# Kernel optimization log

Measured on AMD Instinct MI355X. Metric: run time of the kernel, lower is better.

The kernel has to match this reference:

```python
import jax, jax.numpy as jnp
import numpy as np

B, H, L, P = 16, 256, 8192, 64  # batch, d_input, seq_len, d_state


def setup_inputs() -> dict:
    key = jax.random.key(0)
    k1, k2, k3, k4, k5, k6 = jax.random.split(key, 6)
    u = jax.random.normal(k1, (B, H, L), dtype=jnp.float32)
    # diagonal SSM poles on an annulus inside the unit disk (stable discrete dynamics)
    radius = jax.random.uniform(k2, (P,), minval=0.5, maxval=0.99)
    theta = jax.random.uniform(k3, (P,), minval=0.0, maxval=2.0 * np.pi)
    A_re = (radius * jnp.cos(theta)).astype(jnp.float32)
    A_im = (radius * jnp.sin(theta)).astype(jnp.float32)
    # combined input/output mixing W = C*B, complex (H, P)
    BC_re = (jax.random.normal(k4, (H, P)) / np.sqrt(P)).astype(jnp.float32)
    BC_im = (jax.random.normal(k5, (H, P)) / np.sqrt(P)).astype(jnp.float32)
    # D skip vector: uniform_ring(min_radius=0.0, max_radius=1.0, field='real')
    D = jax.random.uniform(k6, (H,), minval=0.0, maxval=1.0, dtype=jnp.float32)
    return {"u": u, "A_re": A_re, "A_im": A_im, "BC_re": BC_re, "BC_im": BC_im, "D": D}


def reference(u, A_re, A_im, BC_re, BC_im, D):
    # Vandermonde kernel: k[h, l] = sum_p BC[h, p] * A[p]**l, computed stably via exp(l*log A)
    A = jax.lax.complex(A_re, A_im)                      # (P,)
    logA = jnp.log(A)                                    # (P,) complex
    ell = jnp.arange(L, dtype=jnp.float32)               # (L,)
    V = jnp.exp(logA[:, None] * ell[None, :])            # (P, L) complex Vandermonde
    BC = jax.lax.complex(BC_re, BC_im)                   # (H, P)
    k = jnp.einsum('hp,pl->hl', BC, V)                   # (H, L) complex kernel
    # circular FFT convolution (same-length fft/ifft as the torch code)
    u_s = jnp.fft.fft(u, axis=-1)                        # (B, H, L) complex
    k_s = jnp.fft.fft(k, axis=-1)                        # (H, L) complex
    y = jnp.fft.ifft(u_s * k_s[None, :, :], axis=-1).real
    y = y + D[None, :, None] * u                         # D*u skip
    return jnp.tanh(y)                                   # activation (dropout=0 -> identity)
```

## Files before the change

kernel.cpp:

```cpp
#include <hip/hip_runtime.h>
#include <cmath>


typedef _Float16 half8 __attribute__((ext_vector_type(8)));
typedef _Float16 half4v __attribute__((ext_vector_type(4)));
typedef float floatx16 __attribute__((ext_vector_type(16)));

#define NC 64
#define CM 128
#define ROWP 136
#define A2_BYTES ((size_t)256 * 128 * 256 * 2)
#define W_BYTES  ((size_t)128 * 128 * 2)
#define AM_OFF   (A2_BYTES + W_BYTES)

__device__ __forceinline__ float fast_tanh(float x) {
    float e2 = __expf(2.0f * x);
    return 1.0f - 2.0f / (e2 + 1.0f);
}

__global__ void fftconv_prep(const float* __restrict__ A_re, const float* __restrict__ A_im,
                             const float* __restrict__ BC_re, const float* __restrict__ BC_im,
                             const float* __restrict__ Dv, char* __restrict__ ws) {
    __shared__ float rr[64], th[64], br[64], bi[64];
    __shared__ float kk[CM];
    const int h = blockIdx.x, tid = threadIdx.x;
    if (tid < 64) {
        float x = A_re[tid], y = A_im[tid];
        rr[tid] = log2f(sqrtf(x * x + y * y));
        th[tid] = atan2f(y, x);
        br[tid] = BC_re[h * 64 + tid];
        bi[tid] = BC_im[h * 64 + tid];
    }
    __syncthreads();
    if (tid < CM) {
        float d = (float)tid, s = 0.f;
        for (int p = 0; p < 64; ++p) {
            float mag = exp2f(d * rr[p]);
            float ang = d * th[p];
            s += mag * (br[p] * cosf(ang) - bi[p] * sinf(ang));
        }
        kk[tid] = s;
    }
    __syncthreads();
    _Float16* A2 = (_Float16*)ws + (size_t)h * 128 * 256;
    const float Dh = Dv[h];
    for (int idx = tid; idx < 128 * 128; idx += 256) {
        int r = idx >> 7, pc = idx & 127, p = pc & 63;
        float e = (float)(r + 1);
        float mag = exp2f(e * rr[p]);
        float ang = e * th[p];
        float cr = mag * cosf(ang), ci = mag * sinf(ang);
        float val = (pc < 64) ? (br[p] * cr - bi[p] * ci) : -(br[p] * ci + bi[p] * cr);
        A2[r * 256 + pc] = (_Float16)val;
    }
    for (int idx = tid; idx < 128 * 128; idx += 256) {
        int r = idx >> 7, j = idx & 127;
        float v = (j <= r) ? kk[r - j] : 0.f;
        if (j == r) v += Dh;
        A2[r * 256 + CM + j] = (_Float16)v;
    }
    if (h == 0) {
        _Float16* W = (_Float16*)(ws + A2_BYTES);
        for (int idx = tid; idx < 128 * 128; idx += 256) {
            int pc = idx >> 7, j = idx & 127, p = pc & 63;
            float e = (float)(127 - j);
            float mag = exp2f(e * rr[p]);
            float ang = e * th[p];
            float v = (pc < 64) ? mag * cosf(ang) : mag * sinf(ang);
            W[pc * 128 + j] = (_Float16)v;
        }
        if (tid < 64) {
            float mag = exp2f(128.f * rr[tid]);
            float ang = 128.f * th[tid];
            float* aM = (float*)(ws + AM_OFF);
            aM[tid] = mag * cosf(ang);
            aM[64 + tid] = mag * sinf(ang);
        }
    }
}

__global__ __launch_bounds__(256, 2)
void fftconv_main(const float* __restrict__ u, const char* __restrict__ ws,
                  float* __restrict__ out) {
    __shared__ __align__(16) _Float16 u16p[NC * ROWP];
    __shared__ __align__(16) _Float16 S16[NC * ROWP];

    const int tid = threadIdx.x;
    const int lane = tid & 63;
    const int wv = tid >> 6;
    const int h = blockIdx.x >> 4;
    const int bb = blockIdx.x & 15;
    const float* ub = u + ((size_t)bb * 256 + h) * 8192;
    float* yb = out + ((size_t)bb * 256 + h) * 8192;

#pragma unroll
    for (int i = 0; i < 8; ++i) {
        int e4 = i * 256 + tid;
        float4 v = ((const float4*)ub)[e4];
        int el = e4 << 2;
        int c = el >> 7, j = el & 127;
        half4v hv = { (_Float16)v.x, (_Float16)v.y, (_Float16)v.z, (_Float16)v.w };
        *(half4v*)&u16p[c * ROWP + j] = hv;
    }
    __syncthreads();

    const int mrow = (wv << 5) + (lane & 31);
    const int kh = (lane >> 5) << 3;
    const int ncol = lane & 31;

    {
        const _Float16* Wg = (const _Float16*)(ws + A2_BYTES);
        floatx16 acc0 = {}; floatx16 acc1 = {};
#pragma unroll
        for (int s = 0; s < 8; ++s) {
            int k0 = (s << 4) + kh;
            half8 af = *(const half8*)(Wg + mrow * CM + k0);
            half8 b0 = *(const half8*)&u16p[ncol * ROWP + k0];
            half8 b1 = *(const half8*)&u16p[(ncol + 32) * ROWP + k0];
            acc0 = __builtin_amdgcn_mfma_f32_32x32x16_f16(af, b0, acc0, 0, 0, 0);
            acc1 = __builtin_amdgcn_mfma_f32_32x32x16_f16(af, b1, acc1, 0, 0, 0);
        }
        const int pc0 = (wv << 5) + ((lane >> 5) << 2);
#pragma unroll
        for (int g = 0; g < 4; ++g) {
            half4v h0 = { (_Float16)acc0[4 * g + 0], (_Float16)acc0[4 * g + 1],
                          (_Float16)acc0[4 * g + 2], (_Float16)acc0[4 * g + 3] };
            *(half4v*)&S16[ncol * ROWP + pc0 + 8 * g] = h0;
            half4v h1 = { (_Float16)acc1[4 * g + 0], (_Float16)acc1[4 * g + 1],
                          (_Float16)acc1[4 * g + 2], (_Float16)acc1[4 * g + 3] };
            *(half4v*)&S16[(ncol + 32) * ROWP + pc0 + 8 * g] = h1;
        }
    }
    __syncthreads();

    if (wv == 0) {
        const float* aM = (const float*)(ws + AM_OFF);
        const float amr = aM[lane], ami = aM[64 + lane];
        float sr = 0.f, si = 0.f;
#pragma unroll
        for (int c = NC - 8; c < NC; ++c) {
            float xr = (float)S16[c * ROWP + lane];
            float xi = (float)S16[c * ROWP + 64 + lane];
            float nr = fmaf(amr, sr, fmaf(-ami, si, xr));
            float ni = fmaf(amr, si, fmaf(ami, sr, xi));
            sr = nr; si = ni;
        }
#pragma unroll
        for (int c = 0; c < NC; ++c) {
            float xr = (float)S16[c * ROWP + lane];
            float xi = (float)S16[c * ROWP + 64 + lane];
            S16[c * ROWP + lane] = (_Float16)sr;
            S16[c * ROWP + 64 + lane] = (_Float16)si;
            float nr = fmaf(amr, sr, fmaf(-ami, si, xr));
            float ni = fmaf(amr, si, fmaf(ami, sr, xi));
            sr = nr; si = ni;
        }
    }
    __syncthreads();

    {
        const _Float16* Ag = (const _Float16*)ws + ((size_t)h * CM + mrow) * 256;
        floatx16 acc0 = {}; floatx16 acc1 = {};
#pragma unroll
        for (int s = 0; s < 8; ++s) {
            int k0 = (s << 4) + kh;
            half8 af = *(const half8*)(Ag + k0);
            half8 b0 = *(const half8*)&S16[ncol * ROWP + k0];
            half8 b1 = *(const half8*)&S16[(ncol + 32) * ROWP + k0];
            acc0 = __builtin_amdgcn_mfma_f32_32x32x16_f16(af, b0, acc0, 0, 0, 0);
            acc1 = __builtin_amdgcn_mfma_f32_32x32x16_f16(af, b1, acc1, 0, 0, 0);
        }
#pragma unroll
        for (int s = 0; s < 8; ++s) {
            int k0 = (s << 4) + kh;
            half8 af = *(const half8*)(Ag + CM + k0);
            half8 b0 = *(const half8*)&u16p[ncol * ROWP + k0];
            half8 b1 = *(const half8*)&u16p[(ncol + 32) * ROWP + k0];
            acc0 = __builtin_amdgcn_mfma_f32_32x32x16_f16(af, b0, acc0, 0, 0, 0);
            acc1 = __builtin_amdgcn_mfma_f32_32x32x16_f16(af, b1, acc1, 0, 0, 0);
        }
        const int r0 = (wv << 5) + ((lane >> 5) << 2);
#pragma unroll
        for (int g = 0; g < 4; ++g) {
            float4 o0;
            o0.x = fast_tanh(acc0[4 * g + 0]); o0.y = fast_tanh(acc0[4 * g + 1]);
            o0.z = fast_tanh(acc0[4 * g + 2]); o0.w = fast_tanh(acc0[4 * g + 3]);
            *(float4*)(yb + (size_t)ncol * CM + r0 + 8 * g) = o0;
            float4 o1;
            o1.x = fast_tanh(acc1[4 * g + 0]); o1.y = fast_tanh(acc1[4 * g + 1]);
            o1.z = fast_tanh(acc1[4 * g + 2]); o1.w = fast_tanh(acc1[4 * g + 3]);
            *(float4*)(yb + (size_t)(ncol + 32) * CM + r0 + 8 * g) = o1;
        }
    }
}

extern "C" void kernel_launch(void* const* d_in, const int* in_sizes, int n_in,
                              void* d_out, int out_size, void* d_ws, size_t ws_size,
                              hipStream_t stream) {
    const float* u     = (const float*)d_in[0];
    const float* A_re  = (const float*)d_in[1];
    const float* A_im  = (const float*)d_in[2];
    const float* BC_re = (const float*)d_in[3];
    const float* BC_im = (const float*)d_in[4];
    const float* Dv    = (const float*)d_in[5];
    float* out = (float*)d_out;
    char* ws = (char*)d_ws;

    hipLaunchKernelGGL(fftconv_prep, dim3(256), dim3(256), 0, stream,
                       A_re, A_im, BC_re, BC_im, Dv, ws);
    hipLaunchKernelGGL(fftconv_main, dim3(4096), dim3(256), 0, stream,
                       u, ws, out);
}
```

Before: 352.4 us.

## Split each sequence into two halves with halo chunks and raise occupancy

```diff
diff --git a/kernel.cpp b/kernel.cpp
--- a/kernel.cpp
+++ b/kernel.cpp
@@ -6,8 +6,8 @@
 typedef _Float16 half4v __attribute__((ext_vector_type(4)));
 typedef float floatx16 __attribute__((ext_vector_type(16)));
 
-#define NC 64
 #define CM 128
+#define ROWS 40
 #define ROWP 136
 #define A2_BYTES ((size_t)256 * 128 * 256 * 2)
 #define W_BYTES  ((size_t)128 * 128 * 2)
@@ -37,7 +37,7 @@
         for (int p = 0; p < 64; ++p) {
             float mag = exp2f(d * rr[p]);
             float ang = d * th[p];
-            s += mag * (br[p] * cosf(ang) - bi[p] * sinf(ang));
+            s += mag * (br[p] * __cosf(ang) - bi[p] * __sinf(ang));
         }
         kk[tid] = s;
     }
@@ -49,7 +49,7 @@
         float e = (float)(r + 1);
         float mag = exp2f(e * rr[p]);
         float ang = e * th[p];
-        float cr = mag * cosf(ang), ci = mag * sinf(ang);
+        float cr = mag * __cosf(ang), ci = mag * __sinf(ang);
         float val = (pc < 64) ? (br[p] * cr - bi[p] * ci) : -(br[p] * ci + bi[p] * cr);
         A2[r * 256 + pc] = (_Float16)val;
     }
@@ -66,37 +66,41 @@
             float e = (float)(127 - j);
             float mag = exp2f(e * rr[p]);
             float ang = e * th[p];
-            float v = (pc < 64) ? mag * cosf(ang) : mag * sinf(ang);
+            float v = (pc < 64) ? mag * __cosf(ang) : mag * __sinf(ang);
             W[pc * 128 + j] = (_Float16)v;
         }
         if (tid < 64) {
             float mag = exp2f(128.f * rr[tid]);
             float ang = 128.f * th[tid];
             float* aM = (float*)(ws + AM_OFF);
-            aM[tid] = mag * cosf(ang);
-            aM[64 + tid] = mag * sinf(ang);
-        }
-    }
-}
-
-__global__ __launch_bounds__(256, 2)
+            aM[tid] = mag * __cosf(ang);
+            aM[64 + tid] = mag * __sinf(ang);
+        }
+    }
+}
+
+__global__ __launch_bounds__(256, 6)
 void fftconv_main(const float* __restrict__ u, const char* __restrict__ ws,
                   float* __restrict__ out) {
-    __shared__ __align__(16) _Float16 u16p[NC * ROWP];
-    __shared__ __align__(16) _Float16 S16[NC * ROWP];
+    __shared__ __align__(16) _Float16 u16p[ROWS * ROWP];
+    __shared__ __align__(16) _Float16 S16[ROWS * ROWP];
 
     const int tid = threadIdx.x;
     const int lane = tid & 63;
     const int wv = tid >> 6;
-    const int h = blockIdx.x >> 4;
-    const int bb = blockIdx.x & 15;
-    const float* ub = u + ((size_t)bb * 256 + h) * 8192;
-    float* yb = out + ((size_t)bb * 256 + h) * 8192;
-
-#pragma unroll
-    for (int i = 0; i < 8; ++i) {
+    const int hf = blockIdx.x & 1;
+    const int sq = blockIdx.x >> 1;
+    const int h = sq & 255;
+    const float* ub = u + (size_t)sq * 8192;
+    float* yb = out + (size_t)sq * 8192;
+    const int co = hf << 5;
+    const int l0 = ((co << 7) - 1024) & 8191;
+
+#pragma unroll
+    for (int i = 0; i < 5; ++i) {
         int e4 = i * 256 + tid;
-        float4 v = ((const float4*)ub)[e4];
+        int gl = (l0 + (e4 << 2)) & 8191;
+        float4 v = *(const float4*)(ub + gl);
         int el = e4 << 2;
         int c = el >> 7, j = el & 127;
         half4v hv = { (_Float16)v.x, (_Float16)v.y, (_Float16)v.z, (_Float16)v.w };
@@ -107,6 +111,7 @@
     const int mrow = (wv << 5) + (lane & 31);
     const int kh = (lane >> 5) << 3;
     const int ncol = lane & 31;
+    const int r0 = (wv << 5) + ((lane >> 5) << 2);
 
     {
         const _Float16* Wg = (const _Float16*)(ws + A2_BYTES);
@@ -116,19 +121,18 @@
             int k0 = (s << 4) + kh;
             half8 af = *(const half8*)(Wg + mrow * CM + k0);
             half8 b0 = *(const half8*)&u16p[ncol * ROWP + k0];
-            half8 b1 = *(const half8*)&u16p[(ncol + 32) * ROWP + k0];
+            half8 b1 = *(const half8*)&u16p[(8 + ncol) * ROWP + k0];
             acc0 = __builtin_amdgcn_mfma_f32_32x32x16_f16(af, b0, acc0, 0, 0, 0);
             acc1 = __builtin_amdgcn_mfma_f32_32x32x16_f16(af, b1, acc1, 0, 0, 0);
         }
-        const int pc0 = (wv << 5) + ((lane >> 5) << 2);
 #pragma unroll
         for (int g = 0; g < 4; ++g) {
             half4v h0 = { (_Float16)acc0[4 * g + 0], (_Float16)acc0[4 * g + 1],
                           (_Float16)acc0[4 * g + 2], (_Float16)acc0[4 * g + 3] };
-            *(half4v*)&S16[ncol * ROWP + pc0 + 8 * g] = h0;
+            *(half4v*)&S16[ncol * ROWP + r0 + 8 * g] = h0;
             half4v h1 = { (_Float16)acc1[4 * g + 0], (_Float16)acc1[4 * g + 1],
                           (_Float16)acc1[4 * g + 2], (_Float16)acc1[4 * g + 3] };
-            *(half4v*)&S16[(ncol + 32) * ROWP + pc0 + 8 * g] = h1;
+            *(half4v*)&S16[(8 + ncol) * ROWP + r0 + 8 * g] = h1;
         }
     }
     __syncthreads();
@@ -138,7 +142,7 @@
         const float amr = aM[lane], ami = aM[64 + lane];
         float sr = 0.f, si = 0.f;
 #pragma unroll
-        for (int c = NC - 8; c < NC; ++c) {
+        for (int c = 0; c < 8; ++c) {
             float xr = (float)S16[c * ROWP + lane];
             float xi = (float)S16[c * ROWP + 64 + lane];
             float nr = fmaf(amr, sr, fmaf(-ami, si, xr));
@@ -146,7 +150,7 @@
             sr = nr; si = ni;
         }
 #pragma unroll
-        for (int c = 0; c < NC; ++c) {
+        for (int c = 8; c < ROWS; ++c) {
             float xr = (float)S16[c * ROWP + lane];
             float xi = (float)S16[c * ROWP + 64 + lane];
             S16[c * ROWP + lane] = (_Float16)sr;
@@ -160,36 +164,28 @@
 
     {
         const _Float16* Ag = (const _Float16*)ws + ((size_t)h * CM + mrow) * 256;
-        floatx16 acc0 = {}; floatx16 acc1 = {};
+        floatx16 acc = {};
 #pragma unroll
         for (int s = 0; s < 8; ++s) {
             int k0 = (s << 4) + kh;
             half8 af = *(const half8*)(Ag + k0);
-            half8 b0 = *(const half8*)&S16[ncol * ROWP + k0];
-            half8 b1 = *(const half8*)&S16[(ncol + 32) * ROWP + k0];
-            acc0 = __builtin_amdgcn_mfma_f32_32x32x16_f16(af, b0, acc0, 0, 0, 0);
-            acc1 = __builtin_amdgcn_mfma_f32_32x32x16_f16(af, b1, acc1, 0, 0, 0);
+            half8 b = *(const half8*)&S16[(8 + ncol) * ROWP + k0];
+            acc = __builtin_amdgcn_mfma_f32_32x32x16_f16(af, b, acc, 0, 0, 0);
         }
 #pragma unroll
         for (int s = 0; s < 8; ++s) {
             int k0 = (s << 4) + kh;
             half8 af = *(const half8*)(Ag + CM + k0);
-            half8 b0 = *(const half8*)&u16p[ncol * ROWP + k0];
-            half8 b1 = *(const half8*)&u16p[(ncol + 32) * ROWP + k0];
-            acc0 = __builtin_amdgcn_mfma_f32_32x32x16_f16(af, b0, acc0, 0, 0, 0);
-            acc1 = __builtin_amdgcn_mfma_f32_32x32x16_f16(af, b1, acc1, 0, 0, 0);
-        }
-        const int r0 = (wv << 5) + ((lane >> 5) << 2);
+            half8 b = *(const half8*)&u16p[(8 + ncol) * ROWP + k0];
+            acc = __builtin_amdgcn_mfma_f32_32x32x16_f16(af, b, acc, 0, 0, 0);
+        }
+        const int gc = co + ncol;
 #pragma unroll
         for (int g = 0; g < 4; ++g) {
-            float4 o0;
-            o0.x = fast_tanh(acc0[4 * g + 0]); o0.y = fast_tanh(acc0[4 * g + 1]);
-            o0.z = fast_tanh(acc0[4 * g + 2]); o0.w = fast_tanh(acc0[4 * g + 3]);
-            *(float4*)(yb + (size_t)ncol * CM + r0 + 8 * g) = o0;
-            float4 o1;
-            o1.x = fast_tanh(acc1[4 * g + 0]); o1.y = fast_tanh(acc1[4 * g + 1]);
-            o1.z = fast_tanh(acc1[4 * g + 2]); o1.w = fast_tanh(acc1[4 * g + 3]);
-            *(float4*)(yb + (size_t)(ncol + 32) * CM + r0 + 8 * g) = o1;
+            float4 o;
+            o.x = fast_tanh(acc[4 * g + 0]); o.y = fast_tanh(acc[4 * g + 1]);
+            o.z = fast_tanh(acc[4 * g + 2]); o.w = fast_tanh(acc[4 * g + 3]);
+            *(float4*)(yb + (size_t)gc * CM + r0 + 8 * g) = o;
         }
     }
 }
@@ -208,6 +204,6 @@
 
     hipLaunchKernelGGL(fftconv_prep, dim3(256), dim3(256), 0, stream,
                        A_re, A_im, BC_re, BC_im, Dv, ws);
-    hipLaunchKernelGGL(fftconv_main, dim3(4096), dim3(256), 0, stream,
+    hipLaunchKernelGGL(fftconv_main, dim3(8192), dim3(256), 0, stream,
                        u, ws, out);
 }
```

New measurement: 372.3 us. +5.6%, slower.
